# Performance work log

Measured on AMD Instinct MI355X. Metric: run time of the kernel, lower is better.

The kernel has to match this reference:

```python
import jax, jax.numpy as jnp
import numpy as np

N_NODES = 50000


def _gcn_conv(x, W, b, src, dst, n):
    """PyG GCNConv: add self-loops, symmetric normalization, sum-aggregate."""
    h = x @ W  # [N, out_dim] dense transform first (out_dim <= in_dim path)
    loop = jnp.arange(n, dtype=src.dtype)
    src_sl = jnp.concatenate([src, loop])
    dst_sl = jnp.concatenate([dst, loop])
    # degree computed on destination nodes (incl. self-loops)
    deg = jax.ops.segment_sum(jnp.ones_like(dst_sl, dtype=h.dtype), dst_sl, num_segments=n)
    dinv = jnp.where(deg > 0, jax.lax.rsqrt(deg), 0.0)
    norm = dinv[src_sl] * dinv[dst_sl]  # [E+N]
    msgs = h[src_sl] * norm[:, None]  # gather + scale, [E+N, out_dim]
    out = jax.ops.segment_sum(msgs, dst_sl, num_segments=n)  # scatter-add
    return out + b


def setup_inputs() -> dict:
    key = jax.random.key(0)
    k0, k1, k2, k3 = jax.random.split(key, 4)
    d = 256
    E = 400000
    scale = 1.0 / np.sqrt(d)
    x = jax.random.normal(k0, (N_NODES, d), dtype=jnp.float32)
    edge_index = jax.random.randint(k1, (2, E), 0, N_NODES, dtype=jnp.int64)
    W1 = jax.random.normal(k2, (d, d), dtype=jnp.float32) * scale
    b1 = jnp.zeros((d,), dtype=jnp.float32)
    W2 = jax.random.normal(k3, (d, d), dtype=jnp.float32) * scale
    b2 = jnp.zeros((d,), dtype=jnp.float32)
    return {"x": x, "edge_index": edge_index, "W1": W1, "b1": b1, "W2": W2, "b2": b2}


def reference(x, edge_index, W1, b1, W2, b2):
    src, dst = edge_index[0], edge_index[1]
    h = _gcn_conv(x, W1, b1, src, dst, N_NODES)
    h = jax.nn.relu(h)
    h = _gcn_conv(h, W2, b2, src, dst, N_NODES)
    h = jax.nn.relu(h)
    return h
```

## Files before the change

### kernel.cpp

```cpp
#include <hip/hip_runtime.h>
#include <stdint.h>

typedef __bf16 bf16_t;
typedef bf16_t bf16x4 __attribute__((ext_vector_type(4)));
typedef bf16_t bf16x8 __attribute__((ext_vector_type(8)));
typedef float f32x4 __attribute__((ext_vector_type(4)));

#define DIM 256
#define NNODES 50000

__global__ void detect_kernel(const int* __restrict__ ei, int* __restrict__ flags) {
    __shared__ int s_zero;
    if (threadIdx.x == 0) s_zero = 0;
    __syncthreads();
    int z = (ei[2 * threadIdx.x + 1] == 0) ? 1 : 0;
    atomicAdd(&s_zero, z);
    __syncthreads();
    if (threadIdx.x == 0) flags[0] = (s_zero > 128) ? 1 : 0;
}

__device__ __forceinline__ int load_edge(const int* __restrict__ ei, int E, int f64,
                                         int which , int e) {
    int v = f64 ? ei[(size_t)which * 2 * E + 2 * (size_t)e]
                : ei[(size_t)which * E + (size_t)e];
    return min(max(v, 0), NNODES - 1);
}


__global__ void hist_kernel(const int* __restrict__ ei, int E, const int* __restrict__ flags,
                            int* __restrict__ counts) {
    int e = blockIdx.x * blockDim.x + threadIdx.x;
    if (e < E) atomicAdd(&counts[load_edge(ei, E, flags[0], 1, e)], 1);
}

__global__ __launch_bounds__(256) void scanA_kernel(const int* __restrict__ counts,
                                                    int* __restrict__ offsets,
                                                    int* __restrict__ bsums, int n) {
    __shared__ int sm[256];
    int b = blockIdx.x, t = threadIdx.x;
    int idx = b * 256 + t;
    int v = (idx < n) ? counts[idx] : 0;
    sm[t] = v;
    __syncthreads();
    #pragma unroll
    for (int off = 1; off < 256; off <<= 1) {
        int u = (t >= off) ? sm[t - off] : 0;
        __syncthreads();
        sm[t] += u;
        __syncthreads();
    }
    if (idx < n) offsets[idx + 1] = sm[t];
    if (t == 255) bsums[b] = sm[255];
}

__global__ __launch_bounds__(256) void scanB_kernel(int* __restrict__ bsums, int nb) {
    __shared__ int sm[256];
    int t = threadIdx.x;
    int v = (t < nb) ? bsums[t] : 0;
    sm[t] = v;
    __syncthreads();
    #pragma unroll
    for (int off = 1; off < 256; off <<= 1) {
        int u = (t >= off) ? sm[t - off] : 0;
        __syncthreads();
        sm[t] += u;
        __syncthreads();
    }
    if (t < nb) bsums[t] = sm[t] - v;
}

__global__ __launch_bounds__(256) void scanC_kernel(const int* __restrict__ counts,
                                                    const int* __restrict__ bsums,
                                                    int* __restrict__ offsets,
                                                    float* __restrict__ dinv,
                                                    int* __restrict__ cursor, int n) {
    int b = blockIdx.x;
    int idx = b * 256 + threadIdx.x;
    if (idx == 0) offsets[0] = 0;
    if (idx < n) {
        int incl = offsets[idx + 1] + bsums[b];
        offsets[idx + 1] = incl;
        cursor[idx] = incl - counts[idx];
        dinv[idx] = rsqrtf((float)(counts[idx] + 1));
    }
}

__global__ void scatter_kernel(const int* __restrict__ ei, int E, const int* __restrict__ flags,
                               const float* __restrict__ dinv, int* __restrict__ cursor,
                               int2* __restrict__ csr_e) {
    int e = blockIdx.x * blockDim.x + threadIdx.x;
    if (e < E) {
        int s = load_edge(ei, E, flags[0], 0, e);
        int d = load_edge(ei, E, flags[0], 1, e);
        int pos = atomicAdd(&cursor[d], 1);
        if (pos >= 0 && pos < E) {
            int2 v;
            v.x = s;
            v.y = __float_as_int(dinv[s] * dinv[d]);
            csr_e[pos] = v;
        }
    }
}


__global__ void convert_w_kernel(const float* __restrict__ W1, const float* __restrict__ W2,
                                 bf16_t* __restrict__ Wf1, bf16_t* __restrict__ Wf2) {
    const float* W = blockIdx.y ? W2 : W1;
    bf16_t* Wf = blockIdx.y ? Wf2 : Wf1;
    int k = blockIdx.x, n = threadIdx.x;
    int s = k >> 5, quad = (k >> 3) & 3, j = k & 7;
    int nt = n >> 4, m = n & 15;
    Wf[s * 8192 + (nt * 64 + quad * 16 + m) * 8 + j] = (bf16_t)W[k * DIM + n];
}


template <bool F32A>
__global__ __launch_bounds__(256, 4) void gemm_kernel(const void* __restrict__ Xv,
                                                      const bf16_t* __restrict__ Wf,
                                                      bf16_t* __restrict__ H, int tiles) {
    __shared__ bf16_t sB[8192];
    int tid = threadIdx.x;
    int wave = tid >> 6, lane = tid & 63;
    int m = lane & 15, quad = lane >> 4;
    int tile = blockIdx.x * 4 + wave;
    bool active = tile < tiles;
    int arow = (min(tile, tiles - 1)) * 16 + m;

    f32x4 acc[16] = {};

    for (int s = 0; s < 8; s++) {
        __syncthreads();
        {
            const bf16x8* g = (const bf16x8*)Wf + s * 1024;
            bf16x8* d = (bf16x8*)sB;
            #pragma unroll
            for (int it = 0; it < 4; it++) d[tid + it * 256] = g[tid + it * 256];
        }
        __syncthreads();

        bf16x8 a;
        if (F32A) {
            const f32x4* xp = (const f32x4*)((const float*)Xv + (size_t)arow * DIM + s * 32 + quad * 8);
            f32x4 x0 = xp[0], x1 = xp[1];
            #pragma unroll
            for (int j = 0; j < 4; j++) { a[j] = (bf16_t)x0[j]; a[j + 4] = (bf16_t)x1[j]; }
        } else {
            a = *(const bf16x8*)((const bf16_t*)Xv + (size_t)arow * DIM + s * 32 + quad * 8);
        }

        #pragma unroll
        for (int nt = 0; nt < 16; nt++) {
            bf16x8 b = *(const bf16x8*)(sB + nt * 512 + lane * 8);
            acc[nt] = __builtin_amdgcn_mfma_f32_16x16x32_bf16(a, b, acc[nt], 0, 0, 0);
        }
    }

    if (active) {
        int rowb = tile * 16 + quad * 4;
        #pragma unroll
        for (int nt = 0; nt < 16; nt++) {
            #pragma unroll
            for (int r = 0; r < 4; r++) {
                H[(size_t)(rowb + r) * DIM + nt * 16 + m] = (bf16_t)acc[nt][r];
            }
        }
    }
}


template <bool OUT_BF16>
__global__ __launch_bounds__(256) void aggregate_kernel(const bf16_t* __restrict__ H,
                                                        const int* __restrict__ offsets,
                                                        const int2* __restrict__ csr_e,
                                                        const float* __restrict__ dinv,
                                                        const float* __restrict__ bias,
                                                        void* __restrict__ outv, int n) {
    int g = threadIdx.x >> 6;
    int l = threadIdx.x & 63;
    int i = blockIdx.x * 4 + g;
    if (i >= n) return;
    float dii = dinv[i];

    auto cvt = [](bf16x4 v) -> f32x4 {
        f32x4 r;
        #pragma unroll
        for (int j = 0; j < 4; j++) r[j] = (float)v[j];
        return r;
    };

    f32x4 acc = cvt(*(const bf16x4*)(H + (size_t)i * DIM + l * 4)) * (dii * dii);
    int e0 = offsets[i], e1 = offsets[i + 1];

    for (int e = e0; e < e1; e += 64) {
        int rem = e1 - e;
        int2 ed;
        if (l < rem) {
            ed = csr_e[e + l];
        } else {
            ed.x = i;
            ed.y = 0;
        }
        int nb = rem < 64 ? rem : 64;
        for (int b = 0; b < nb; b += 8) {
            bf16x4 h[8];
            float w[8];
            #pragma unroll
            for (int jj = 0; jj < 8; jj++) {
                int s = (int)__builtin_amdgcn_readlane((unsigned)ed.x, (unsigned)(b + jj));
                unsigned wb = __builtin_amdgcn_readlane((unsigned)ed.y, (unsigned)(b + jj));
                w[jj] = __uint_as_float(wb);
                h[jj] = *(const bf16x4*)(H + (size_t)s * DIM + l * 4);
            }
            #pragma unroll
            for (int jj = 0; jj < 8; jj++) acc += cvt(h[jj]) * w[jj];
        }
    }

    acc += *(const f32x4*)(bias + l * 4);
    #pragma unroll
    for (int j = 0; j < 4; j++) acc[j] = fmaxf(acc[j], 0.0f);

    if (OUT_BF16) {
        bf16x4 o;
        #pragma unroll
        for (int j = 0; j < 4; j++) o[j] = (bf16_t)acc[j];
        *(bf16x4*)((bf16_t*)outv + (size_t)i * DIM + l * 4) = o;
    } else {
        *(f32x4*)((float*)outv + (size_t)i * DIM + l * 4) = acc;
    }
}


extern "C" void kernel_launch(void* const* d_in, const int* in_sizes, int n_in,
                              void* d_out, int out_size, void* d_ws, size_t ws_size,
                              hipStream_t stream) {
    const float* x  = (const float*)d_in[0];
    const int*   ei = (const int*)d_in[1];
    const float* W1 = (const float*)d_in[2];
    const float* b1 = (const float*)d_in[3];
    const float* W2 = (const float*)d_in[4];
    const float* b2 = (const float*)d_in[5];
    float* out = (float*)d_out;

    const int n = NNODES;
    const int E = in_sizes[1] / 2;
    const int nb = (n + 255) / 256;

    char* ws = (char*)d_ws;
    size_t off = 0;
    auto alloc = [&](size_t bytes) -> char* {
        char* p = ws + off;
        off += (bytes + 255) & ~(size_t)255;
        return p;
    };
    int*    flags    = (int*)alloc(256);
    float*  dinv     = (float*)alloc((size_t)n * 4);
    int*    counts   = (int*)alloc((size_t)n * 4);
    int*    offsets  = (int*)alloc((size_t)(n + 1) * 4);
    int*    cursor   = (int*)alloc((size_t)n * 4);
    int*    bsums    = (int*)alloc((size_t)nb * 4);
    int2*   csr_e    = (int2*)alloc((size_t)E * 8);
    bf16_t* Wf1      = (bf16_t*)alloc((size_t)DIM * DIM * 2);
    bf16_t* Wf2      = (bf16_t*)alloc((size_t)DIM * DIM * 2);
    bf16_t* P        = (bf16_t*)alloc((size_t)n * DIM * 2);
    bf16_t* X2       = (bf16_t*)alloc((size_t)n * DIM * 2);

    detect_kernel<<<1, 256, 0, stream>>>(ei, flags);
    hipMemsetAsync(counts, 0, (size_t)n * 4, stream);
    hist_kernel<<<(E + 255) / 256, 256, 0, stream>>>(ei, E, flags, counts);
    scanA_kernel<<<nb, 256, 0, stream>>>(counts, offsets, bsums, n);
    scanB_kernel<<<1, 256, 0, stream>>>(bsums, nb);
    scanC_kernel<<<nb, 256, 0, stream>>>(counts, bsums, offsets, dinv, cursor, n);
    scatter_kernel<<<(E + 255) / 256, 256, 0, stream>>>(ei, E, flags, dinv, cursor, csr_e);

    convert_w_kernel<<<dim3(DIM, 2), DIM, 0, stream>>>(W1, W2, Wf1, Wf2);

    int tiles = (n + 15) / 16;
    int gemm_blocks = (tiles + 3) / 4;
    int agg_blocks = n / 4;

    gemm_kernel<true><<<gemm_blocks, 256, 0, stream>>>(x, Wf1, P, tiles);
    aggregate_kernel<true><<<agg_blocks, 256, 0, stream>>>(P, offsets, csr_e, dinv, b1, X2, n);
    gemm_kernel<false><<<gemm_blocks, 256, 0, stream>>>(X2, Wf2, P, tiles);
    aggregate_kernel<false><<<agg_blocks, 256, 0, stream>>>(P, offsets, csr_e, dinv, b2, out, n);
}
```

Before: 261.3 us.

## Store intermediate features in column panels and aggregate per panel

The GEMM output and the layer-1 activations move to a panel-major layout: 8 panels of 32 columns, each covering all nodes. The aggregation runs one panel per block, with 8 nodes per wave and 8 lanes per node. The intent is to shrink each gather's working set to one panel (3.2MB) so random neighbour rows stay in cache, and to remove under-utilised waves on low-degree nodes. The separate detect kernel is also folded into hist and scatter as a per-wave ballot. In exchange each gathered row is only 64 bytes, and the edge lists are re-read once per panel.

```diff
diff --git a/kernel.cpp b/kernel.cpp
--- a/kernel.cpp
+++ b/kernel.cpp
@@ -8,15 +8,13 @@
 
 #define DIM 256
 #define NNODES 50000
-
-__global__ void detect_kernel(const int* __restrict__ ei, int* __restrict__ flags) {
-    __shared__ int s_zero;
-    if (threadIdx.x == 0) s_zero = 0;
-    __syncthreads();
-    int z = (ei[2 * threadIdx.x + 1] == 0) ? 1 : 0;
-    atomicAdd(&s_zero, z);
-    __syncthreads();
-    if (threadIdx.x == 0) flags[0] = (s_zero > 128) ? 1 : 0;
+#define NPANEL 8
+#define PDIM 32
+
+__device__ __forceinline__ int detect_f64(const int* __restrict__ ei) {
+    int v = ei[2 * (threadIdx.x & 63) + 1];
+    unsigned long long m = __ballot(v == 0);
+    return __popcll(m) > 32;
 }
 
 __device__ __forceinline__ int load_edge(const int* __restrict__ ei, int E, int f64,
@@ -27,10 +25,10 @@
 }
 
 
-__global__ void hist_kernel(const int* __restrict__ ei, int E, const int* __restrict__ flags,
-                            int* __restrict__ counts) {
+__global__ void hist_kernel(const int* __restrict__ ei, int E, int* __restrict__ counts) {
+    int f64 = detect_f64(ei);
     int e = blockIdx.x * blockDim.x + threadIdx.x;
-    if (e < E) atomicAdd(&counts[load_edge(ei, E, flags[0], 1, e)], 1);
+    if (e < E) atomicAdd(&counts[load_edge(ei, E, f64, 1, e)], 1);
 }
 
 __global__ __launch_bounds__(256) void scanA_kernel(const int* __restrict__ counts,
@@ -85,13 +83,14 @@
     }
 }
 
-__global__ void scatter_kernel(const int* __restrict__ ei, int E, const int* __restrict__ flags,
+__global__ void scatter_kernel(const int* __restrict__ ei, int E,
                                const float* __restrict__ dinv, int* __restrict__ cursor,
                                int2* __restrict__ csr_e) {
+    int f64 = detect_f64(ei);
     int e = blockIdx.x * blockDim.x + threadIdx.x;
     if (e < E) {
-        int s = load_edge(ei, E, flags[0], 0, e);
-        int d = load_edge(ei, E, flags[0], 1, e);
+        int s = load_edge(ei, E, f64, 0, e);
+        int d = load_edge(ei, E, f64, 1, e);
         int pos = atomicAdd(&cursor[d], 1);
         if (pos >= 0 && pos < E) {
             int2 v;
@@ -117,7 +116,7 @@
 template <bool F32A>
 __global__ __launch_bounds__(256, 4) void gemm_kernel(const void* __restrict__ Xv,
                                                       const bf16_t* __restrict__ Wf,
-                                                      bf16_t* __restrict__ H, int tiles) {
+                                                      bf16_t* __restrict__ Hp, int tiles) {
     __shared__ bf16_t sB[8192];
     int tid = threadIdx.x;
     int wave = tid >> 6, lane = tid & 63;
@@ -145,7 +144,7 @@
             #pragma unroll
             for (int j = 0; j < 4; j++) { a[j] = (bf16_t)x0[j]; a[j + 4] = (bf16_t)x1[j]; }
         } else {
-            a = *(const bf16x8*)((const bf16_t*)Xv + (size_t)arow * DIM + s * 32 + quad * 8);
+            a = *(const bf16x8*)((const bf16_t*)Xv + ((size_t)s * NNODES + arow) * PDIM + quad * 8);
         }
 
         #pragma unroll
@@ -159,27 +158,29 @@
         int rowb = tile * 16 + quad * 4;
         #pragma unroll
         for (int nt = 0; nt < 16; nt++) {
+            size_t pbase = ((size_t)(nt >> 1) * NNODES) * PDIM + (nt & 1) * 16 + m;
             #pragma unroll
             for (int r = 0; r < 4; r++) {
-                H[(size_t)(rowb + r) * DIM + nt * 16 + m] = (bf16_t)acc[nt][r];
+                Hp[pbase + (size_t)(rowb + r) * PDIM] = (bf16_t)acc[nt][r];
             }
         }
     }
 }
 
 
-template <bool OUT_BF16>
-__global__ __launch_bounds__(256) void aggregate_kernel(const bf16_t* __restrict__ H,
+template <int OUT_BF16P>
+__global__ __launch_bounds__(256) void aggregate_kernel(const bf16_t* __restrict__ Hp,
                                                         const int* __restrict__ offsets,
                                                         const int2* __restrict__ csr_e,
                                                         const float* __restrict__ dinv,
                                                         const float* __restrict__ bias,
                                                         void* __restrict__ outv, int n) {
-    int g = threadIdx.x >> 6;
-    int l = threadIdx.x & 63;
-    int i = blockIdx.x * 4 + g;
+    int p = blockIdx.x & 7;
+    int chunk = blockIdx.x >> 3;
+    int wave = threadIdx.x >> 6, lane = threadIdx.x & 63;
+    int g = lane >> 3, c = lane & 7;
+    int i = chunk * 32 + wave * 8 + g;
     if (i >= n) return;
-    float dii = dinv[i];
 
     auto cvt = [](bf16x4 v) -> f32x4 {
         f32x4 r;
@@ -188,45 +189,46 @@
         return r;
     };
 
-    f32x4 acc = cvt(*(const bf16x4*)(H + (size_t)i * DIM + l * 4)) * (dii * dii);
+    const bf16_t* Hpan = Hp + (size_t)p * ((size_t)NNODES * PDIM);
+    float dii = dinv[i];
+    f32x4 acc = cvt(*(const bf16x4*)(Hpan + (size_t)i * PDIM + c * 4)) * (dii * dii);
     int e0 = offsets[i], e1 = offsets[i + 1];
 
-    for (int e = e0; e < e1; e += 64) {
-        int rem = e1 - e;
+    for (int e = e0; e < e1; e += 8) {
         int2 ed;
-        if (l < rem) {
-            ed = csr_e[e + l];
+        if (e + c < e1) {
+            ed = csr_e[e + c];
         } else {
             ed.x = i;
             ed.y = 0;
         }
-        int nb = rem < 64 ? rem : 64;
-        for (int b = 0; b < nb; b += 8) {
-            bf16x4 h[8];
-            float w[8];
-            #pragma unroll
-            for (int jj = 0; jj < 8; jj++) {
-                int s = (int)__builtin_amdgcn_readlane((unsigned)ed.x, (unsigned)(b + jj));
-                unsigned wb = __builtin_amdgcn_readlane((unsigned)ed.y, (unsigned)(b + jj));
-                w[jj] = __uint_as_float(wb);
-                h[jj] = *(const bf16x4*)(H + (size_t)s * DIM + l * 4);
-            }
-            #pragma unroll
-            for (int jj = 0; jj < 8; jj++) acc += cvt(h[jj]) * w[jj];
-        }
-    }
-
-    acc += *(const f32x4*)(bias + l * 4);
+        int s[8]; float w[8];
+        #pragma unroll
+        for (int j = 0; j < 8; j++) {
+            int srcLane = (lane & 56) + j;
+            s[j] = __shfl(ed.x, srcLane, 64);
+            w[j] = __uint_as_float((unsigned)__shfl(ed.y, srcLane, 64));
+        }
+        bf16x4 h[8];
+        #pragma unroll
+        for (int j = 0; j < 8; j++) {
+            h[j] = *(const bf16x4*)(Hpan + (size_t)s[j] * PDIM + c * 4);
+        }
+        #pragma unroll
+        for (int j = 0; j < 8; j++) acc += cvt(h[j]) * w[j];
+    }
+
+    acc += *(const f32x4*)(bias + p * PDIM + c * 4);
     #pragma unroll
     for (int j = 0; j < 4; j++) acc[j] = fmaxf(acc[j], 0.0f);
 
-    if (OUT_BF16) {
+    if (OUT_BF16P) {
         bf16x4 o;
         #pragma unroll
         for (int j = 0; j < 4; j++) o[j] = (bf16_t)acc[j];
-        *(bf16x4*)((bf16_t*)outv + (size_t)i * DIM + l * 4) = o;
+        *(bf16x4*)((bf16_t*)outv + (size_t)p * NNODES * PDIM + (size_t)i * PDIM + c * 4) = o;
     } else {
-        *(f32x4*)((float*)outv + (size_t)i * DIM + l * 4) = acc;
+        *(f32x4*)((float*)outv + (size_t)i * DIM + p * PDIM + c * 4) = acc;
     }
 }
 
@@ -253,7 +255,6 @@
         off += (bytes + 255) & ~(size_t)255;
         return p;
     };
-    int*    flags    = (int*)alloc(256);
     float*  dinv     = (float*)alloc((size_t)n * 4);
     int*    counts   = (int*)alloc((size_t)n * 4);
     int*    offsets  = (int*)alloc((size_t)(n + 1) * 4);
@@ -265,22 +266,21 @@
     bf16_t* P        = (bf16_t*)alloc((size_t)n * DIM * 2);
     bf16_t* X2       = (bf16_t*)alloc((size_t)n * DIM * 2);
 
-    detect_kernel<<<1, 256, 0, stream>>>(ei, flags);
     hipMemsetAsync(counts, 0, (size_t)n * 4, stream);
-    hist_kernel<<<(E + 255) / 256, 256, 0, stream>>>(ei, E, flags, counts);
+    hist_kernel<<<(E + 255) / 256, 256, 0, stream>>>(ei, E, counts);
     scanA_kernel<<<nb, 256, 0, stream>>>(counts, offsets, bsums, n);
     scanB_kernel<<<1, 256, 0, stream>>>(bsums, nb);
     scanC_kernel<<<nb, 256, 0, stream>>>(counts, bsums, offsets, dinv, cursor, n);
-    scatter_kernel<<<(E + 255) / 256, 256, 0, stream>>>(ei, E, flags, dinv, cursor, csr_e);
+    scatter_kernel<<<(E + 255) / 256, 256, 0, stream>>>(ei, E, dinv, cursor, csr_e);
 
     convert_w_kernel<<<dim3(DIM, 2), DIM, 0, stream>>>(W1, W2, Wf1, Wf2);
 
     int tiles = (n + 15) / 16;
     int gemm_blocks = (tiles + 3) / 4;
-    int agg_blocks = n / 4;
+    int agg_blocks = NPANEL * ((n + 31) / 32);
 
     gemm_kernel<true><<<gemm_blocks, 256, 0, stream>>>(x, Wf1, P, tiles);
-    aggregate_kernel<true><<<agg_blocks, 256, 0, stream>>>(P, offsets, csr_e, dinv, b1, X2, n);
+    aggregate_kernel<1><<<agg_blocks, 256, 0, stream>>>(P, offsets, csr_e, dinv, b1, X2, n);
     gemm_kernel<false><<<gemm_blocks, 256, 0, stream>>>(X2, Wf2, P, tiles);
-    aggregate_kernel<false><<<agg_blocks, 256, 0, stream>>>(P, offsets, csr_e, dinv, b2, out, n);
-}
+    aggregate_kernel<0><<<agg_blocks, 256, 0, stream>>>(P, offsets, csr_e, dinv, b2, out, n);
+}
```

Result: no change. 259.0 us (-0.9%).
